# Kernel optimization log

Hardware: AMD Instinct MI355X
Metric: run time of the kernel (lower is better)

## Reference

```python
import jax, jax.numpy as jnp
import numpy as np

EPS = 1e-5  # torch BatchNorm default eps
RF = 4      # receptive_field for blocks=3, layers=1, kernel_size=2


def _conv1x1(x, W, b):
    # x: [B,C,N,T], W: [O,C], b: [O] -> [B,O,N,T]
    return jnp.einsum('bcnt,oc->bont', x, W) + b[None, :, None, None]


def _bn(x, gamma, beta, mean, var):
    # eval-mode BatchNorm2d over channel axis 1 (pure affine with running stats)
    inv = gamma * jax.lax.rsqrt(var + EPS)
    return x * inv[None, :, None, None] + (beta - mean * inv)[None, :, None, None]


def _nconv(x, A):
    # torch.einsum('ncvl,vw->ncwl', x, A)
    return jnp.einsum('bcvt,vw->bcwt', x, A)


def setup_inputs() -> dict:
    key = jax.random.key(0)
    ks = jax.random.split(key, 32)
    B, Cin, N, T = 64, 2, 512, 12
    D = 128            # d_model == d_ff (required: output_bn is BatchNorm2d(d_model) on skip)
    n_steps = 3        # blocks * layers
    n_gc = n_steps - 1 # graph convs actually used (loop breaks before last)

    inp = {}
    inp['x'] = jax.random.normal(ks[0], (B, Cin, N, T), dtype=jnp.float32)
    # row-scaled dense adjacency so repeated hops stay numerically sane
    inp['adj'] = jax.random.uniform(ks[1], (N, N), dtype=jnp.float32) / N

    inp['W_start'] = jax.random.normal(ks[2], (D, Cin), dtype=jnp.float32) / np.sqrt(Cin)
    inp['b_start'] = jax.random.normal(ks[3], (D,), dtype=jnp.float32) * 0.02

    inp['W_skip'] = jax.random.normal(ks[4], (n_steps, D, D), dtype=jnp.float32) / np.sqrt(D)
    inp['b_skip'] = jax.random.normal(ks[5], (n_steps, D), dtype=jnp.float32) * 0.02

    inp['W_gc'] = jax.random.normal(ks[6], (n_gc, D, 3 * D), dtype=jnp.float32) / np.sqrt(3 * D)
    inp['b_gc'] = jax.random.normal(ks[7], (n_gc, D), dtype=jnp.float32) * 0.02

    inp['gc_gamma'] = 1.0 + 0.1 * jax.random.normal(ks[8], (n_gc, D), dtype=jnp.float32)
    inp['gc_beta'] = 0.1 * jax.random.normal(ks[9], (n_gc, D), dtype=jnp.float32)
    inp['gc_mean'] = 0.1 * jax.random.normal(ks[10], (n_gc, D), dtype=jnp.float32)
    inp['gc_var'] = jax.random.uniform(ks[11], (n_gc, D), dtype=jnp.float32, minval=0.5, maxval=1.5)

    inp['bn_gamma'] = 1.0 + 0.1 * jax.random.normal(ks[12], (n_gc, D), dtype=jnp.float32)
    inp['bn_beta'] = 0.1 * jax.random.normal(ks[13], (n_gc, D), dtype=jnp.float32)
    inp['bn_mean'] = 0.1 * jax.random.normal(ks[14], (n_gc, D), dtype=jnp.float32)
    inp['bn_var'] = jax.random.uniform(ks[15], (n_gc, D), dtype=jnp.float32, minval=0.5, maxval=1.5)

    inp['ob_gamma'] = 1.0 + 0.1 * jax.random.normal(ks[16], (D,), dtype=jnp.float32)
    inp['ob_beta'] = 0.1 * jax.random.normal(ks[17], (D,), dtype=jnp.float32)
    inp['ob_mean'] = 0.1 * jax.random.normal(ks[18], (D,), dtype=jnp.float32)
    inp['ob_var'] = jax.random.uniform(ks[19], (D,), dtype=jnp.float32, minval=0.5, maxval=1.5)
    return inp


def reference(x, adj, W_start, b_start, W_skip, b_skip, W_gc, b_gc,
              gc_gamma, gc_beta, gc_mean, gc_var,
              bn_gamma, bn_beta, bn_mean, bn_var,
              ob_gamma, ob_beta, ob_mean, ob_var):
    # start conv: [B,Cin,N,T] -> [B,D,N,T]
    x = _conv1x1(x, W_start, b_start)
    T = x.shape[3]
    if T < RF:  # static shape check, matches F.pad(x, (RF-T, 0, 0, 0))
        x = jnp.pad(x, ((0, 0), (0, 0), (0, 0), (RF - T, 0)))

    n_steps = W_skip.shape[0]
    skip = None
    for i in range(n_steps):  # fixed small layer count
        residual = x
        s = _conv1x1(x, W_skip[i], b_skip[i])          # [B,Dff,N,T]
        skip = s if skip is None else skip + s          # all T equal (1x1 convs only)
        if i == n_steps - 1:
            break
        x1 = _nconv(x, adj)
        x2 = _nconv(x1, adj)
        h = jnp.concatenate([x, x1, x2], axis=1)        # [B,3D,N,T]
        h = _conv1x1(h, W_gc[i], b_gc[i])               # [B,D,N,T]
        h = _bn(h, gc_gamma[i], gc_beta[i], gc_mean[i], gc_var[i])
        x = h + residual
        x = _bn(x, bn_gamma[i], bn_beta[i], bn_mean[i], bn_var[i])

    out = _bn(skip, ob_gamma, ob_beta, ob_mean, ob_var)  # output_bn
    return jnp.swapaxes(out, 1, 3)                       # x.transpose(1, -1): [B,T,N,D]
```

## Files before the change

kernel.cpp:

```cpp
#include <hip/hip_runtime.h>

#define TT 12
#define NN 512
#define CD 128
#define SLICE (CD*NN)
#define NSL 768

typedef __attribute__((ext_vector_type(8))) short short8;
typedef __attribute__((ext_vector_type(4))) float f32x4;
typedef unsigned short u16;

__device__ __forceinline__ u16 f2bf(float f){
    union { float f; unsigned u; } v; v.f = f;
    return (u16)((v.u + 0x7FFFu + ((v.u >> 16) & 1u)) >> 16);
}
__device__ __forceinline__ float bf2f(u16 h){
    union { unsigned u; float f; } v; v.u = ((unsigned)h) << 16;
    return v.f;
}

__global__ __launch_bounds__(256) void k_adjT(const float* __restrict__ src,
        u16* __restrict__ DT){
    int idx = blockIdx.x*256 + threadIdx.x;
    int w = idx >> 9, v = idx & (NN-1);
    DT[(size_t)w*NN + v] = f2bf(src[(size_t)v*NN + w]);
}

__global__ __launch_bounds__(256) void k_a2(const float* __restrict__ adj,
        float* __restrict__ A2){
    int u = blockIdx.x >> 1;
    int w = (blockIdx.x & 1)*256 + threadIdx.x;
    float acc = 0.f;
    for (int v = 0; v < NN; v++) acc += adj[(size_t)u*NN+v] * adj[(size_t)v*NN+w];
    A2[(size_t)u*NN+w] = acc;
}

__global__ __launch_bounds__(256) void k_cast(const float* __restrict__ src,
        u16* __restrict__ dst){
    int i = blockIdx.x*256 + threadIdx.x;
    dst[i] = f2bf(src[i]);
}

__global__ __launch_bounds__(256) void k_start(const float* __restrict__ x0,
        const float* __restrict__ Wst, const float* __restrict__ bst,
        u16* __restrict__ Sbf, u16* __restrict__ S0T, const int s0){
    __shared__ float Lv[2*64];
    __shared__ __align__(16) short Tt[64*136];
    const int t  = threadIdx.x;
    const int sl = blockIdx.x >> 3;
    const int n0 = (blockIdx.x & 7) * 64;
    const int s = s0 + sl;
    const int b = s / TT, tt = s - b*TT;
    if (t < 128) {
        int ci = t >> 6, nl2 = t & 63;
        Lv[ci*64 + nl2] = x0[(size_t)((b*2 + ci)*NN + n0 + nl2)*TT + tt];
    }
    __syncthreads();
    const int nl = t & 63;
    const int dg = (t >> 6) * 32;
    const float v0 = Lv[nl], v1 = Lv[64 + nl];
    const size_t base = (size_t)sl * SLICE;
    #pragma unroll 4
    for (int dd = 0; dd < 32; dd++) {
        int d = dg + dd;
        float val = Wst[2*d]*v0 + Wst[2*d+1]*v1 + bst[d];
        u16 bv = f2bf(val);
        Sbf[base + (size_t)d*NN + n0 + nl] = bv;
        Tt[nl*136 + d] = (short)bv;
    }
    __syncthreads();
    #pragma unroll
    for (int q = 0; q < 4; q++) {
        int id = t + q*256;
        int row = id >> 4, c0 = (id & 15) * 8;
        *(short8*)(S0T + base + (size_t)(n0 + row)*CD + c0) =
            *(const short8*)(Tt + row*136 + c0);
    }
}

__global__ __launch_bounds__(256) void k_hop2(const u16* __restrict__ AT,
        const u16* __restrict__ A2T, const u16* __restrict__ Sbf,
        u16* __restrict__ X1T, u16* __restrict__ X2T){
    __shared__ __align__(16) short As[128*72];
    __shared__ __align__(16) short Bs[128*72];
    const int t    = threadIdx.x;
    const int sl   = blockIdx.x >> 3;
    const int r    = blockIdx.x & 7;
    const u16* M   = (r & 4) ? A2T : AT;
    u16* DT        = (r & 4) ? X2T : X1T;
    const int wb   = (r & 3) * 128;
    const int lane = t & 63, wid = t >> 6;
    const int wr   = (wid >> 1) * 64, wc = (wid & 1) * 64;
    const int r0   = t >> 3, co = (t & 7) * 8;
    const u16* Ss  = Sbf + (size_t)sl * SLICE;
    f32x4 acc[4][4] = {};
    for (int kb = 0; kb < NN; kb += 64) {
        #pragma unroll
        for (int p = 0; p < 4; p++) {
            int row = p*32 + r0;
            *(short8*)(As + row*72 + co) = *(const short8*)(Ss + (size_t)row*NN + kb + co);
            *(short8*)(Bs + row*72 + co) = *(const short8*)(M  + (size_t)(wb+row)*NN + kb + co);
        }
        __syncthreads();
        #pragma unroll
        for (int ks = 0; ks < 64; ks += 32) {
            const int kg = ks + ((lane >> 4) << 3);
            const int lr = lane & 15;
            short8 af[4], bfr[4];
            #pragma unroll
            for (int i = 0; i < 4; i++) af[i]  = *(const short8*)(As + (wr + i*16 + lr)*72 + kg);
            #pragma unroll
            for (int j = 0; j < 4; j++) bfr[j] = *(const short8*)(Bs + (wc + j*16 + lr)*72 + kg);
            #pragma unroll
            for (int i = 0; i < 4; i++)
                #pragma unroll
                for (int j = 0; j < 4; j++)
                    acc[i][j] = __builtin_amdgcn_mfma_f32_16x16x32_bf16(af[i], bfr[j], acc[i][j], 0, 0, 0);
        }
        __syncthreads();
    }
    const int lr = lane & 15, lh = lane >> 4;
    u16* Dp = DT + (size_t)sl * SLICE;
    #pragma unroll
    for (int i = 0; i < 4; i++)
        #pragma unroll
        for (int j = 0; j < 4; j++) {
            const int c0 = wr + i*16 + lh*4;
            const int w  = wb + wc + j*16 + lr;
            f32x4 v = acc[i][j];
            ushort4 q;
            q.x = f2bf(v[0]); q.y = f2bf(v[1]); q.z = f2bf(v[2]); q.w = f2bf(v[3]);
            *(ushort4*)(Dp + (size_t)w*CD + c0) = q;
        }
}

__global__ __launch_bounds__(256) void k_gc_mx(
        const u16* __restrict__ ST, const u16* __restrict__ X1T, const u16* __restrict__ X2T,
        const u16* __restrict__ Wg, const float* __restrict__ bias,
        u16* __restrict__ Sbf, u16* __restrict__ SnT,
        const float* __restrict__ gg, const float* __restrict__ gb,
        const float* __restrict__ gm, const float* __restrict__ gv,
        const float* __restrict__ bg, const float* __restrict__ bb,
        const float* __restrict__ bm, const float* __restrict__ bv){
    __shared__ __align__(16) short As[128*72];
    __shared__ __align__(16) short Bs[128*72];
    __shared__ float Cst[5*128];
    const int t    = threadIdx.x;
    const int sl   = blockIdx.x >> 2;
    const int nb   = (blockIdx.x & 3) * 128;
    const int lane = t & 63, wid = t >> 6;
    const int wr   = (wid >> 1) * 64, wc = (wid & 1) * 64;
    const int r0   = t >> 3, co = (t & 7) * 8;
    if (t < 128) {
        float ig = gg[t] * rsqrtf(gv[t] + 1e-5f);
        float ib = bg[t] * rsqrtf(bv[t] + 1e-5f);
        Cst[t]       = ig;
        Cst[128 + t] = gb[t] - gm[t]*ig;
        Cst[256 + t] = ib;
        Cst[384 + t] = bb[t] - bm[t]*ib;
        Cst[512 + t] = bias[t];
    }
    const u16* srcs[3] = { ST  + (size_t)sl*SLICE,
                           X1T + (size_t)sl*SLICE,
                           X2T + (size_t)sl*SLICE };
    f32x4 acc[4][4] = {};
    #pragma unroll
    for (int kb = 0; kb < 384; kb += 64) {
        const u16* Sp = srcs[kb >> 7];
        const int  kc = kb & 127;
        #pragma unroll
        for (int p = 0; p < 4; p++) {
            int row = p*32 + r0;
            *(short8*)(As + row*72 + co) = *(const short8*)(Wg + (size_t)row*384 + kb + co);
            *(short8*)(Bs + row*72 + co) = *(const short8*)(Sp + (size_t)(nb+row)*CD + kc + co);
        }
        __syncthreads();
        #pragma unroll
        for (int ks = 0; ks < 64; ks += 32) {
            const int kg = ks + ((lane >> 4) << 3);
            const int lr = lane & 15;
            short8 af[4], bfr[4];
            #pragma unroll
            for (int i = 0; i < 4; i++) af[i]  = *(const short8*)(As + (wr + i*16 + lr)*72 + kg);
            #pragma unroll
            for (int j = 0; j < 4; j++) bfr[j] = *(const short8*)(Bs + (wc + j*16 + lr)*72 + kg);
            #pragma unroll
            for (int i = 0; i < 4; i++)
                #pragma unroll
                for (int j = 0; j < 4; j++)
                    acc[i][j] = __builtin_amdgcn_mfma_f32_16x16x32_bf16(af[i], bfr[j], acc[i][j], 0, 0, 0);
        }
        __syncthreads();
    }
    const int lr = lane & 15, lh = lane >> 4;
    const size_t base = (size_t)sl * SLICE;
    const u16* Rs = srcs[0];
    u16* Sn = SnT + base;
    #pragma unroll
    for (int i = 0; i < 4; i++) {
        const int o0 = wr + i*16 + lh*4;
        float ig4[4], cg4[4], ib4[4], cb4[4], h04[4];
        #pragma unroll
        for (int r2 = 0; r2 < 4; r2++) {
            int o = o0 + r2;
            ig4[r2] = Cst[o]; cg4[r2] = Cst[128+o]; ib4[r2] = Cst[256+o];
            cb4[r2] = Cst[384+o]; h04[r2] = Cst[512+o];
        }
        #pragma unroll
        for (int j = 0; j < 4; j++) {
            const int nl = wc + j*16 + lr;
            ushort4 r4 = *(const ushort4*)(Rs + (size_t)(nb + nl)*CD + o0);
            f32x4 a = acc[i][j];
            u16 bq[4];
            bq[0] = f2bf(ib4[0]*( ig4[0]*(a[0] + h04[0]) + cg4[0] + bf2f(r4.x) ) + cb4[0]);
            bq[1] = f2bf(ib4[1]*( ig4[1]*(a[1] + h04[1]) + cg4[1] + bf2f(r4.y) ) + cb4[1]);
            bq[2] = f2bf(ib4[2]*( ig4[2]*(a[2] + h04[2]) + cg4[2] + bf2f(r4.z) ) + cb4[2]);
            bq[3] = f2bf(ib4[3]*( ig4[3]*(a[3] + h04[3]) + cg4[3] + bf2f(r4.w) ) + cb4[3]);
            ushort4 q; q.x = bq[0]; q.y = bq[1]; q.z = bq[2]; q.w = bq[3];
            *(ushort4*)(Sn + (size_t)(nb + nl)*CD + o0) = q;
            #pragma unroll
            for (int r2 = 0; r2 < 4; r2++)
                Sbf[base + (size_t)(o0 + r2)*NN + nb + nl] = bq[r2];
        }
    }
}

__global__ __launch_bounds__(256) void k_skip_fused(
        const u16* __restrict__ S0T, const u16* __restrict__ S1T, const u16* __restrict__ S2T,
        const u16* __restrict__ Wsb, const float* __restrict__ bsk,
        const float* __restrict__ og, const float* __restrict__ obt,
        const float* __restrict__ om, const float* __restrict__ ov,
        float* __restrict__ out, const int s0){
    __shared__ __align__(16) short As[128*72];
    __shared__ __align__(16) short Bs[128*72];
    __shared__ float Cst[3*128];
    const int t    = threadIdx.x;
    const int sl   = blockIdx.x >> 2;
    const int nbt  = (blockIdx.x & 3) * 128;
    const int lane = t & 63, wid = t >> 6;
    const int wr   = (wid >> 1) * 64, wc = (wid & 1) * 64;
    const int r0   = t >> 3, co = (t & 7) * 8;
    if (t < 128) {
        float inv = og[t] * rsqrtf(ov[t] + 1e-5f);
        Cst[t]       = inv;
        Cst[128 + t] = obt[t] - om[t]*inv;
        Cst[256 + t] = bsk[t] + bsk[CD + t] + bsk[2*CD + t];
    }
    const u16* srcs[3] = { S0T + (size_t)sl*SLICE,
                           S1T + (size_t)sl*SLICE,
                           S2T + (size_t)sl*SLICE };
    f32x4 acc[4][4] = {};
    #pragma unroll
    for (int kb = 0; kb < 384; kb += 64) {
        const u16* Sp = srcs[kb >> 7];
        const int  ph = kb >> 7;
        const int  kc = kb & 127;
        #pragma unroll
        for (int p = 0; p < 4; p++) {
            int row = p*32 + r0;
            *(short8*)(As + row*72 + co) = *(const short8*)(Wsb + (size_t)ph*CD*CD + (size_t)row*CD + kc + co);
            *(short8*)(Bs + row*72 + co) = *(const short8*)(Sp + (size_t)(nbt+row)*CD + kc + co);
        }
        __syncthreads();
        #pragma unroll
        for (int ks = 0; ks < 64; ks += 32) {
            const int kg = ks + ((lane >> 4) << 3);
            const int lr = lane & 15;
            short8 af[4], bfr[4];
            #pragma unroll
            for (int i = 0; i < 4; i++) af[i]  = *(const short8*)(As + (wr + i*16 + lr)*72 + kg);
            #pragma unroll
            for (int j = 0; j < 4; j++) bfr[j] = *(const short8*)(Bs + (wc + j*16 + lr)*72 + kg);
            #pragma unroll
            for (int i = 0; i < 4; i++)
                #pragma unroll
                for (int j = 0; j < 4; j++)
                    acc[i][j] = __builtin_amdgcn_mfma_f32_16x16x32_bf16(af[i], bfr[j], acc[i][j], 0, 0, 0);
        }
        __syncthreads();
    }
    const int lr = lane & 15, lh = lane >> 4;
    float* Op = out + (size_t)(s0 + sl) * SLICE;
    #pragma unroll
    for (int i = 0; i < 4; i++) {
        const int o0 = wr + i*16 + lh*4;
        float ao4[4], c04[4], sb4[4];
        #pragma unroll
        for (int r2 = 0; r2 < 4; r2++) {
            int o = o0 + r2;
            ao4[r2] = Cst[o]; c04[r2] = Cst[128+o]; sb4[r2] = Cst[256+o];
        }
        #pragma unroll
        for (int j = 0; j < 4; j++) {
            const int n = nbt + wc + j*16 + lr;
            f32x4 v = acc[i][j];
            float4 q;
            q.x = ao4[0]*(v[0] + sb4[0]) + c04[0];
            q.y = ao4[1]*(v[1] + sb4[1]) + c04[1];
            q.z = ao4[2]*(v[2] + sb4[2]) + c04[2];
            q.w = ao4[3]*(v[3] + sb4[3]) + c04[3];
            *(float4*)(Op + (size_t)n*CD + o0) = q;
        }
    }
}

extern "C" void kernel_launch(void* const* d_in, const int* in_sizes, int n_in,
                              void* d_out, int out_size, void* d_ws, size_t ws_size,
                              hipStream_t stream) {
    const float* x0   = (const float*)d_in[0];
    const float* adj  = (const float*)d_in[1];
    const float* Wst  = (const float*)d_in[2];
    const float* bst  = (const float*)d_in[3];
    const float* Wsk  = (const float*)d_in[4];
    const float* bsk  = (const float*)d_in[5];
    const float* Wgc  = (const float*)d_in[6];
    const float* bgc  = (const float*)d_in[7];
    const float* gg   = (const float*)d_in[8];
    const float* gb   = (const float*)d_in[9];
    const float* gm   = (const float*)d_in[10];
    const float* gv   = (const float*)d_in[11];
    const float* bg   = (const float*)d_in[12];
    const float* bb   = (const float*)d_in[13];
    const float* bm   = (const float*)d_in[14];
    const float* bv   = (const float*)d_in[15];
    const float* og   = (const float*)d_in[16];
    const float* obt  = (const float*)d_in[17];
    const float* om   = (const float*)d_in[18];
    const float* ov   = (const float*)d_in[19];
    float* out = (float*)d_out;

    float* A2f   = (float*)d_ws;
    u16*   AT    = (u16*)(A2f + NN*NN);
    u16*   A2T   = AT  + NN*NN;
    u16*   Wskbf = A2T + NN*NN;
    u16*   Wgcbf = Wskbf + 3*CD*CD;
    char*  pend  = (char*)(Wgcbf + 2*CD*384);
    size_t goff  = ((size_t)(pend - (char*)d_ws) + 255) & ~(size_t)255;

    static const int divs[] = {768,384,256,192,128,96,64,48,32,24,16,12,8,6,4,3,2,1};
    const size_t perSlice = 6*(size_t)SLICE*2;
    int SC = 1;
    for (int di = 0; di < 18; di++) {
        if (goff + (size_t)divs[di]*perSlice <= ws_size) { SC = divs[di]; break; }
    }
    u16* Sbf = (u16*)((char*)d_ws + goff);
    u16* S0T = Sbf + (size_t)SC*SLICE;
    u16* S1T = S0T + (size_t)SC*SLICE;
    u16* S2T = S1T + (size_t)SC*SLICE;
    u16* X1T = S2T + (size_t)SC*SLICE;
    u16* X2T = X1T + (size_t)SC*SLICE;

    k_adjT<<<(NN*NN)/256, 256, 0, stream>>>(adj, AT);
    k_a2  <<<NN*2,        256, 0, stream>>>(adj, A2f);
    k_adjT<<<(NN*NN)/256, 256, 0, stream>>>(A2f, A2T);
    k_cast<<<(3*CD*CD)/256,  256, 0, stream>>>(Wsk, Wskbf);
    k_cast<<<(2*CD*384)/256, 256, 0, stream>>>(Wgc, Wgcbf);

    for (int s0 = 0; s0 < NSL; s0 += SC) {
        k_start<<<SC*8, 256, 0, stream>>>(x0, Wst, bst, Sbf, S0T, s0);
        for (int i = 0; i < 2; i++) {
            k_hop2<<<SC*8, 256, 0, stream>>>(AT, A2T, Sbf, X1T, X2T);
            k_gc_mx<<<SC*4, 256, 0, stream>>>(
                (i ? S1T : S0T), X1T, X2T,
                Wgcbf + (size_t)i*CD*384, bgc + i*CD,
                Sbf, (i ? S2T : S1T),
                gg + i*CD, gb + i*CD, gm + i*CD, gv + i*CD,
                bg + i*CD, bb + i*CD, bm + i*CD, bv + i*CD);
        }
        k_skip_fused<<<SC*4, 256, 0, stream>>>(S0T, S1T, S2T, Wskbf, bsk,
                                               og, obt, om, ov, out, s0);
    }
}
```

Baseline: 1.034 ms.

## Stage GEMM tiles with direct global-to-LDS loads and XOR swizzle

Replaces register-staged global-to-shared copies in the three MFMA GEMM kernels with direct global_load_lds transfers into unpadded 64-wide LDS tiles, using an XOR swizzle on the 16-byte column chunk to avoid bank conflicts instead of row padding. The hop2 kernel also remaps block indices so blocks sharing the same adjacency matrix and row band are scheduled together, aiming for better L2 reuse. The change is meant to cut VGPR traffic and load-store instruction overhead during tile staging. It depends on the builtin's LDS addressing semantics (per-wave base plus lane offset) matching the layout the swizzle assumes.

```diff
diff --git a/kernel.cpp b/kernel.cpp
--- a/kernel.cpp
+++ b/kernel.cpp
@@ -17,6 +17,23 @@
 __device__ __forceinline__ float bf2f(u16 h){
     union { unsigned u; float f; } v; v.u = ((unsigned)h) << 16;
     return v.f;
+}
+
+__device__ __forceinline__ void gload16(const void* g, void* l){
+    __builtin_amdgcn_global_load_lds(
+        (const __attribute__((address_space(1))) unsigned int*)g,
+        (__attribute__((address_space(3))) unsigned int*)l, 16, 0, 0);
+}
+
+__device__ __forceinline__ void stage128x64(short* lds, const char* gbase,
+        const int rowstride, const int t){
+    const int rr  = t >> 3;
+    const int swz = (((t & 7) ^ (rr & 7)) << 4);
+    short* lw = lds + ((t >> 6) << 9);
+    #pragma unroll
+    for (int p = 0; p < 4; p++){
+        gload16(gbase + (size_t)(p*32 + rr)*rowstride + swz, lw + p*2048);
+    }
 }
 
 __global__ __launch_bounds__(256) void k_adjT(const float* __restrict__ src,
@@ -81,36 +98,36 @@
 __global__ __launch_bounds__(256) void k_hop2(const u16* __restrict__ AT,
         const u16* __restrict__ A2T, const u16* __restrict__ Sbf,
         u16* __restrict__ X1T, u16* __restrict__ X2T){
-    __shared__ __align__(16) short As[128*72];
-    __shared__ __align__(16) short Bs[128*72];
-    const int t    = threadIdx.x;
-    const int sl   = blockIdx.x >> 3;
-    const int r    = blockIdx.x & 7;
-    const u16* M   = (r & 4) ? A2T : AT;
-    u16* DT        = (r & 4) ? X2T : X1T;
-    const int wb   = (r & 3) * 128;
+    __shared__ __align__(16) short As[128*64];
+    __shared__ __align__(16) short Bs[128*64];
+    const int t = threadIdx.x;
+    int work = blockIdx.x;
+    const int nblk = gridDim.x;
+    if (!(nblk & 7)) work = (work & 7) * (nblk >> 3) + (work >> 3);
+    const int sl = work >> 3;
+    const int r  = work & 7;
+    const u16* M = (r & 4) ? A2T : AT;
+    u16* DT      = (r & 4) ? X2T : X1T;
+    const int wb = (r & 3) * 128;
     const int lane = t & 63, wid = t >> 6;
     const int wr   = (wid >> 1) * 64, wc = (wid & 1) * 64;
-    const int r0   = t >> 3, co = (t & 7) * 8;
     const u16* Ss  = Sbf + (size_t)sl * SLICE;
+    const int lr = lane & 15;
+    const int kh = (lane >> 4) << 3;
+    const int xr = (lr & 7) << 3;
     f32x4 acc[4][4] = {};
     for (int kb = 0; kb < NN; kb += 64) {
-        #pragma unroll
-        for (int p = 0; p < 4; p++) {
-            int row = p*32 + r0;
-            *(short8*)(As + row*72 + co) = *(const short8*)(Ss + (size_t)row*NN + kb + co);
-            *(short8*)(Bs + row*72 + co) = *(const short8*)(M  + (size_t)(wb+row)*NN + kb + co);
-        }
+        stage128x64(As, (const char*)Ss + (size_t)kb*2, NN*2, t);
+        stage128x64(Bs, (const char*)(M + (size_t)wb*NN) + (size_t)kb*2, NN*2, t);
         __syncthreads();
         #pragma unroll
         for (int ks = 0; ks < 64; ks += 32) {
-            const int kg = ks + ((lane >> 4) << 3);
-            const int lr = lane & 15;
+            const int kx = (ks + kh) ^ xr;
             short8 af[4], bfr[4];
             #pragma unroll
-            for (int i = 0; i < 4; i++) af[i]  = *(const short8*)(As + (wr + i*16 + lr)*72 + kg);
-            #pragma unroll
-            for (int j = 0; j < 4; j++) bfr[j] = *(const short8*)(Bs + (wc + j*16 + lr)*72 + kg);
+            for (int i = 0; i < 4; i++) af[i]  = *(const short8*)(As + (wr + i*16 + lr)*64 + kx);
+            #pragma unroll
+            for (int j = 0; j < 4; j++) bfr[j] = *(const short8*)(Bs + (wc + j*16 + lr)*64 + kx);
             #pragma unroll
             for (int i = 0; i < 4; i++)
                 #pragma unroll
@@ -119,7 +136,7 @@
         }
         __syncthreads();
     }
-    const int lr = lane & 15, lh = lane >> 4;
+    const int lh = lane >> 4;
     u16* Dp = DT + (size_t)sl * SLICE;
     #pragma unroll
     for (int i = 0; i < 4; i++)
@@ -142,15 +159,14 @@
         const float* __restrict__ gm, const float* __restrict__ gv,
         const float* __restrict__ bg, const float* __restrict__ bb,
         const float* __restrict__ bm, const float* __restrict__ bv){
-    __shared__ __align__(16) short As[128*72];
-    __shared__ __align__(16) short Bs[128*72];
+    __shared__ __align__(16) short As[128*64];
+    __shared__ __align__(16) short Bs[128*64];
     __shared__ float Cst[5*128];
     const int t    = threadIdx.x;
     const int sl   = blockIdx.x >> 2;
     const int nb   = (blockIdx.x & 3) * 128;
     const int lane = t & 63, wid = t >> 6;
     const int wr   = (wid >> 1) * 64, wc = (wid & 1) * 64;
-    const int r0   = t >> 3, co = (t & 7) * 8;
     if (t < 128) {
         float ig = gg[t] * rsqrtf(gv[t] + 1e-5f);
         float ib = bg[t] * rsqrtf(bv[t] + 1e-5f);
@@ -163,27 +179,25 @@
     const u16* srcs[3] = { ST  + (size_t)sl*SLICE,
                            X1T + (size_t)sl*SLICE,
                            X2T + (size_t)sl*SLICE };
+    const int lr = lane & 15;
+    const int kh = (lane >> 4) << 3;
+    const int xr = (lr & 7) << 3;
     f32x4 acc[4][4] = {};
     #pragma unroll
     for (int kb = 0; kb < 384; kb += 64) {
         const u16* Sp = srcs[kb >> 7];
         const int  kc = kb & 127;
-        #pragma unroll
-        for (int p = 0; p < 4; p++) {
-            int row = p*32 + r0;
-            *(short8*)(As + row*72 + co) = *(const short8*)(Wg + (size_t)row*384 + kb + co);
-            *(short8*)(Bs + row*72 + co) = *(const short8*)(Sp + (size_t)(nb+row)*CD + kc + co);
-        }
+        stage128x64(As, (const char*)Wg + (size_t)kb*2, 384*2, t);
+        stage128x64(Bs, (const char*)(Sp + (size_t)nb*CD) + (size_t)kc*2, CD*2, t);
         __syncthreads();
         #pragma unroll
         for (int ks = 0; ks < 64; ks += 32) {
-            const int kg = ks + ((lane >> 4) << 3);
-            const int lr = lane & 15;
+            const int kx = (ks + kh) ^ xr;
             short8 af[4], bfr[4];
             #pragma unroll
-            for (int i = 0; i < 4; i++) af[i]  = *(const short8*)(As + (wr + i*16 + lr)*72 + kg);
-            #pragma unroll
-            for (int j = 0; j < 4; j++) bfr[j] = *(const short8*)(Bs + (wc + j*16 + lr)*72 + kg);
+            for (int i = 0; i < 4; i++) af[i]  = *(const short8*)(As + (wr + i*16 + lr)*64 + kx);
+            #pragma unroll
+            for (int j = 0; j < 4; j++) bfr[j] = *(const short8*)(Bs + (wc + j*16 + lr)*64 + kx);
             #pragma unroll
             for (int i = 0; i < 4; i++)
                 #pragma unroll
@@ -192,7 +206,7 @@
         }
         __syncthreads();
     }
-    const int lr = lane & 15, lh = lane >> 4;
+    const int lh = lane >> 4;
     const size_t base = (size_t)sl * SLICE;
     const u16* Rs = srcs[0];
     u16* Sn = SnT + base;
@@ -231,15 +245,14 @@
         const float* __restrict__ og, const float* __restrict__ obt,
         const float* __restrict__ om, const float* __restrict__ ov,
         float* __restrict__ out, const int s0){
-    __shared__ __align__(16) short As[128*72];
-    __shared__ __align__(16) short Bs[128*72];
+    __shared__ __align__(16) short As[128*64];
+    __shared__ __align__(16) short Bs[128*64];
     __shared__ float Cst[3*128];
     const int t    = threadIdx.x;
     const int sl   = blockIdx.x >> 2;
     const int nbt  = (blockIdx.x & 3) * 128;
     const int lane = t & 63, wid = t >> 6;
     const int wr   = (wid >> 1) * 64, wc = (wid & 1) * 64;
-    const int r0   = t >> 3, co = (t & 7) * 8;
     if (t < 128) {
         float inv = og[t] * rsqrtf(ov[t] + 1e-5f);
         Cst[t]       = inv;
@@ -249,28 +262,26 @@
     const u16* srcs[3] = { S0T + (size_t)sl*SLICE,
                            S1T + (size_t)sl*SLICE,
                            S2T + (size_t)sl*SLICE };
+    const int lr = lane & 15;
+    const int kh = (lane >> 4) << 3;
+    const int xr = (lr & 7) << 3;
     f32x4 acc[4][4] = {};
     #pragma unroll
     for (int kb = 0; kb < 384; kb += 64) {
         const u16* Sp = srcs[kb >> 7];
         const int  ph = kb >> 7;
         const int  kc = kb & 127;
-        #pragma unroll
-        for (int p = 0; p < 4; p++) {
-            int row = p*32 + r0;
-            *(short8*)(As + row*72 + co) = *(const short8*)(Wsb + (size_t)ph*CD*CD + (size_t)row*CD + kc + co);
-            *(short8*)(Bs + row*72 + co) = *(const short8*)(Sp + (size_t)(nbt+row)*CD + kc + co);
-        }
+        stage128x64(As, (const char*)(Wsb + (size_t)ph*CD*CD) + (size_t)kc*2, CD*2, t);
+        stage128x64(Bs, (const char*)(Sp + (size_t)nbt*CD) + (size_t)kc*2, CD*2, t);
         __syncthreads();
         #pragma unroll
         for (int ks = 0; ks < 64; ks += 32) {
-            const int kg = ks + ((lane >> 4) << 3);
-            const int lr = lane & 15;
+            const int kx = (ks + kh) ^ xr;
             short8 af[4], bfr[4];
             #pragma unroll
-            for (int i = 0; i < 4; i++) af[i]  = *(const short8*)(As + (wr + i*16 + lr)*72 + kg);
-            #pragma unroll
-            for (int j = 0; j < 4; j++) bfr[j] = *(const short8*)(Bs + (wc + j*16 + lr)*72 + kg);
+            for (int i = 0; i < 4; i++) af[i]  = *(const short8*)(As + (wr + i*16 + lr)*64 + kx);
+            #pragma unroll
+            for (int j = 0; j < 4; j++) bfr[j] = *(const short8*)(Bs + (wc + j*16 + lr)*64 + kx);
             #pragma unroll
             for (int i = 0; i < 4; i++)
                 #pragma unroll
@@ -279,7 +290,7 @@
         }
         __syncthreads();
     }
-    const int lr = lane & 15, lh = lane >> 4;
+    const int lh = lane >> 4;
     float* Op = out + (size_t)(s0 + sl) * SLICE;
     #pragma unroll
     for (int i = 0; i < 4; i++) {
```

New measurement: 988.2 us. -4.5%, faster.
